# Optimization experiments

Hardware: AMD Instinct MI355X
Metric: run time of the kernel (lower is better)

Reference implementation:

```python
import jax, jax.numpy as jnp
import numpy as np

B, T, D, H = 8, 2048, 512, 128

def setup_inputs() -> dict:
    key = jax.random.key(0)
    ks = jax.random.split(key, 8)
    s = lambda fan_in: 1.0 / np.sqrt(fan_in)
    return {
        "x": jax.random.normal(ks[0], (B, T, D), jnp.float32),
        "prediction": jax.random.normal(ks[1], (B, T, D), jnp.float32),
        "Wq": jax.random.uniform(ks[2], (D, H), jnp.float32, -s(D), s(D)),
        "bq": jnp.zeros((H,), jnp.float32),
        "Wk": jax.random.uniform(ks[3], (D, H), jnp.float32, -s(D), s(D)),
        "bk": jnp.zeros((H,), jnp.float32),
        "Wv": jax.random.uniform(ks[4], (D, D), jnp.float32, -s(D), s(D)),
        "bv": jnp.zeros((D,), jnp.float32),
        "Wf": jax.random.uniform(ks[5], (2 * D, D), jnp.float32, -s(2 * D), s(2 * D)),
        "bf": jnp.zeros((D,), jnp.float32),
    }

def reference(x, prediction, Wq, bq, Wk, bk, Wv, bv, Wf, bf):
    # q,k: [B,T,H]; v: [B,T,D]
    q = jnp.einsum('btd,dh->bth', prediction, Wq) + bq
    k = jnp.einsum('btd,dh->bth', x, Wk) + bk
    v = jnp.einsum('btd,de->bte', x, Wv) + bv
    # unscaled attention scores [B,T,T]
    scores = jnp.einsum('bth,bsh->bts', q, k)
    attn = jax.nn.softmax(scores, axis=-1)
    attended = jnp.einsum('bts,bsd->btd', attn, v)
    fusion_input = jnp.concatenate([prediction, attended], axis=-1)  # [B,T,2D]
    return jax.nn.sigmoid(jnp.einsum('btf,fd->btd', fusion_input, Wf) + bf)
```

## Files before the change

kernel.cpp:

```cpp
#include <hip/hip_runtime.h>
#include <hip/hip_bf16.h>


#define APF_B 8
#define APF_T 2048
#define APF_D 512
#define APF_H 128
#define APF_M (APF_B * APF_T)

#define GSWZ(row) ((((row) >> 1) & 3) << 3)

typedef unsigned short u16;
typedef __attribute__((ext_vector_type(8))) short short8;
typedef __attribute__((ext_vector_type(4))) float f32x4;
typedef __attribute__((ext_vector_type(16))) float f32x16;

static __device__ __forceinline__ u16 f2bf(float x) {
    union { float f; unsigned int u; } cv;
    cv.f = x;
    unsigned int u = cv.u + 0x7FFFu + ((cv.u >> 16) & 1u);
    return (u16)(u >> 16);
}
static __device__ __forceinline__ u16 f2bf_hw(float x) {
    union { __hip_bfloat16 h; u16 u; } cv;
    cv.h = __float2bfloat16(x);
    return cv.u;
}

static __device__ __forceinline__ void load16_lds(const u16* g, u16* l) {
    __builtin_amdgcn_global_load_lds(
        (const __attribute__((address_space(1))) unsigned int*)g,
        (__attribute__((address_space(3))) unsigned int*)l,
        16, 0, 0);
}

template <int N>
static __device__ __forceinline__ void bar_keep() {
    if constexpr (N == 0)
        asm volatile("s_waitcnt vmcnt(0) lgkmcnt(0)\ns_barrier" ::: "memory");
    else if constexpr (N == 4)
        asm volatile("s_waitcnt vmcnt(4) lgkmcnt(0)\ns_barrier" ::: "memory");
    else if constexpr (N == 8)
        asm volatile("s_waitcnt vmcnt(8) lgkmcnt(0)\ns_barrier" ::: "memory");
}

static __device__ __forceinline__ f32x16 zero16() {
    f32x16 v;
#pragma unroll
    for (int i = 0; i < 16; ++i) v[i] = 0.f;
    return v;
}

__global__ __launch_bounds__(256) void prep_w(
    const float* __restrict__ Wq, u16* __restrict__ WqT,
    const float* __restrict__ Wk, u16* __restrict__ WkT,
    const float* __restrict__ Wv, u16* __restrict__ WvT,
    const float* __restrict__ Wf, u16* __restrict__ WfT)
{
    __shared__ float tile[64][65];
    int b = blockIdx.x;
    const float* src; u16* dst; int K, N;
    if (b < 16)      { src = Wq; dst = WqT; K = 512;  N = 128; }
    else if (b < 32) { b -= 16; src = Wk; dst = WkT; K = 512;  N = 128; }
    else if (b < 96) { b -= 32; src = Wv; dst = WvT; K = 512;  N = 512; }
    else             { b -= 96; src = Wf; dst = WfT; K = 1024; N = 512; }
    const int ntN = N >> 6;
    const int k0 = (b / ntN) * 64, n0 = (b % ntN) * 64;

    const int tid = threadIdx.x;
#pragma unroll
    for (int rep = 0; rep < 4; ++rep) {
        const int r = (tid >> 4) + rep * 16;
        const int c = (tid & 15) * 4;
        const float4 v = *(const float4*)&src[(long)(k0 + r) * N + n0 + c];
        tile[r][c] = v.x; tile[r][c + 1] = v.y;
        tile[r][c + 2] = v.z; tile[r][c + 3] = v.w;
    }
    __syncthreads();
#pragma unroll
    for (int rep = 0; rep < 2; ++rep) {
        const int rn = (tid >> 3) + rep * 32;
        const int ck = (tid & 7) * 8;
        short8 o;
#pragma unroll
        for (int j = 0; j < 8; ++j)
            o[j] = (short)f2bf_hw(tile[ck + j][rn]);
        *(short8*)&dst[(long)(n0 + rn) * K + k0 + ck] = o;
    }
}

template <int ADT, int BDT, int EPI, int BIASM, int VBLK>
static __device__ __forceinline__ void gemm_body(
    u16 (&smA)[2][4096], u16 (&smB)[2][4096],
    const void* Ap, long lda,
    const void* Bp, long ldb,
    const float* bias, void* Cp, long ldc, int K,
    long row0, long col0, const float* Cadd)
{
    const int tid  = threadIdx.x;
    const int lane = tid & 63;
    const int wid  = tid >> 6;
    const int wr   = wid >> 1;
    const int wc   = wid & 1;

    f32x4 acc[4][4];
#pragma unroll
    for (int i = 0; i < 4; ++i)
#pragma unroll
        for (int j = 0; j < 4; ++j)
            acc[i][j] = (f32x4){0.f, 0.f, 0.f, 0.f};

    const int lrow = (lane >> 4) * 4;
    const int lcol = lane & 15;
    const int q8   = (lane >> 4) * 8;

    float4 ra[2][2], rb[2][2];

    auto loadA = [&](int kb) {
        if (ADT == 1) {
            const float* Af = (const float*)Ap;
#pragma unroll
            for (int rep = 0; rep < 2; ++rep) {
                const int c = tid + rep * 256;
                const int rr = c >> 2, kc = (c & 3) * 8;
                const float* ga = Af + (row0 + rr) * lda + kb + kc;
                ra[rep][0] = *(const float4*)ga;
                ra[rep][1] = *(const float4*)(ga + 4);
            }
        }
    };
    auto loadB = [&](int kb) {
        if (BDT == 1) {
            const float* Bf = (const float*)Bp;
#pragma unroll
            for (int rep = 0; rep < 2; ++rep) {
                const int c = tid + rep * 256;
                const int rr = c >> 2, kc = (c & 3) * 8;
                const float* gb = Bf + (col0 + rr) * ldb + kb + kc;
                rb[rep][0] = *(const float4*)gb;
                rb[rep][1] = *(const float4*)(gb + 4);
            }
        }
    };
    auto dmaA = [&](int buf, int kb) {
        if (ADT == 0) {
            const u16* Ab = (const u16*)Ap;
#pragma unroll
            for (int rep = 0; rep < 2; ++rep) {
                const int c = tid + rep * 256;
                const int rr = c >> 2, kc = (c & 3) * 8;
                const int wbase = (wid * 64 + rep * 256) * 8;
                load16_lds(Ab + (row0 + rr) * lda + kb + (kc ^ GSWZ(rr)),
                           &smA[buf][wbase]);
            }
        }
    };
    auto dmaB = [&](int buf, int kb) {
        if (BDT == 0) {
            const u16* Bb = (const u16*)Bp;
#pragma unroll
            for (int rep = 0; rep < 2; ++rep) {
                const int c = tid + rep * 256;
                const int rr = c >> 2, kc = (c & 3) * 8;
                const int wbase = (wid * 64 + rep * 256) * 8;
                load16_lds(Bb + (col0 + rr) * ldb + kb + (kc ^ GSWZ(rr)),
                           &smB[buf][wbase]);
            }
        }
    };
    auto cvt8 = [&](const float4& a, const float4& b) {
        short8 v;
        v[0] = (short)f2bf_hw(a.x); v[1] = (short)f2bf_hw(a.y);
        v[2] = (short)f2bf_hw(a.z); v[3] = (short)f2bf_hw(a.w);
        v[4] = (short)f2bf_hw(b.x); v[5] = (short)f2bf_hw(b.y);
        v[6] = (short)f2bf_hw(b.z); v[7] = (short)f2bf_hw(b.w);
        return v;
    };
    auto writeA = [&](int buf) {
        if (ADT == 1) {
#pragma unroll
            for (int rep = 0; rep < 2; ++rep) {
                const int c = tid + rep * 256;
                *(short8*)&smA[buf][(c * 8) ^ GSWZ(c >> 2)] =
                    cvt8(ra[rep][0], ra[rep][1]);
            }
        }
    };
    auto writeB = [&](int buf) {
        if (BDT == 1) {
#pragma unroll
            for (int rep = 0; rep < 2; ++rep) {
                const int c = tid + rep * 256;
                *(short8*)&smB[buf][(c * 8) ^ GSWZ(c >> 2)] =
                    cvt8(rb[rep][0], rb[rep][1]);
            }
        }
    };

    constexpr int NREG = (ADT == 1 ? 4 : 0) + (BDT == 1 ? 4 : 0);

    const int NT = K / 32;
    loadA(0); loadB(0);
    writeA(0); writeB(0);
    dmaA(0, 0); dmaB(0, 0);

    int cur = 0;
    for (int t = 0; t < NT; ++t) {
        const int kb2 = (t + 1) * 32;
        if (t + 1 < NT) {
            loadA(kb2); loadB(kb2);
            bar_keep<NREG>();
            dmaA(cur ^ 1, kb2); dmaB(cur ^ 1, kb2);
        } else {
            bar_keep<0>();
        }

        short8 av[4], bv4[4];
#pragma unroll
        for (int ti = 0; ti < 4; ++ti) {
            const int arow = wr * 64 + ti * 16 + lcol;
            av[ti] = *(const short8*)&smA[cur][arow * 32 + (q8 ^ GSWZ(arow))];
        }
#pragma unroll
        for (int tj = 0; tj < 4; ++tj) {
            const int brow = wc * 64 + tj * 16 + lcol;
            bv4[tj] = *(const short8*)&smB[cur][brow * 32 + (q8 ^ GSWZ(brow))];
        }

#pragma unroll
        for (int ti = 0; ti < 4; ++ti)
#pragma unroll
            for (int tj = 0; tj < 4; ++tj)
                acc[ti][tj] = __builtin_amdgcn_mfma_f32_16x16x32_bf16(
                    av[ti], bv4[tj], acc[ti][tj], 0, 0, 0);

        if (t + 1 < NT) { writeA(cur ^ 1); writeB(cur ^ 1); }
        cur ^= 1;
    }

#pragma unroll
    for (int ti = 0; ti < 4; ++ti) {
        const long m0t = row0 + wr * 64 + ti * 16 + lrow;
#pragma unroll
        for (int tj = 0; tj < 4; ++tj) {
            const long n = col0 + wc * 64 + tj * 16 + lcol;
            const float bn = (BIASM == 0 && bias != nullptr) ? bias[n] : 0.f;
            if (EPI == 0) {
                u16* C = (u16*)Cp;
#pragma unroll
                for (int r = 0; r < 4; ++r) {
                    const long m = m0t + r;
                    const float bm = (BIASM == 1) ? bias[m] : bn;
                    long idx;
                    if (VBLK) {
                        idx = ((((m >> 5) * 256) + (n >> 3)) << 8) +
                              ((m & 31) << 3) + (n & 7);
                    } else {
                        idx = m * ldc + n;
                    }
                    C[idx] = f2bf(acc[ti][tj][r] + bm);
                }
            } else if (EPI == 2) {
                float* C = (float*)Cp;
#pragma unroll
                for (int r = 0; r < 4; ++r) {
                    const float val = acc[ti][tj][r] + bn;
                    C[(m0t + r) * ldc + n] = 1.0f / (1.0f + expf(-val));
                }
            } else if (EPI == 3) {
                float* C = (float*)Cp;
#pragma unroll
                for (int r = 0; r < 4; ++r)
                    C[(m0t + r) * ldc + n] = acc[ti][tj][r] + bn;
            } else {
                float* C = (float*)Cp;
#pragma unroll
                for (int r = 0; r < 4; ++r) {
                    const float val = acc[ti][tj][r] + Cadd[(m0t + r) * ldc + n];
                    C[(m0t + r) * ldc + n] = 1.0f / (1.0f + expf(-val));
                }
            }
        }
    }
}

__global__ __launch_bounds__(256, 3) void mid_gemms(
    const float* __restrict__ x, const float* __restrict__ pred,
    const u16* __restrict__ WqT, const u16* __restrict__ WkT,
    const u16* __restrict__ WvT, const u16* __restrict__ WfT,
    const float* __restrict__ bq, const float* __restrict__ bk,
    const float* __restrict__ bv, const float* __restrict__ bfu,
    u16* __restrict__ qb, u16* __restrict__ kbuf, u16* __restrict__ vTb,
    float* __restrict__ Cpre)
{
    __shared__ u16 smA[2][4096];
    __shared__ u16 smB[2][4096];

    const int bid = blockIdx.x;
    if (bid < 256) {
        const int zz = bid >> 7, by = bid & 127;
        gemm_body<1, 0, 0, 0, 0>(smA, smB,
            zz ? (const void*)x : (const void*)pred, APF_D,
            zz ? WkT : WqT, APF_D,
            zz ? bk : bq, zz ? (void*)kbuf : (void*)qb, APF_H, APF_D,
            (long)by * 128, 0, nullptr);
    } else if (bid < 768) {
        const int t = bid - 256;
        const int zz = t >> 6, rem = t & 63;
        const int bx = rem & 15, by = rem >> 4;
        gemm_body<0, 1, 0, 1, 1>(smA, smB,
            WvT, APF_D,
            (const void*)(x + (long)zz * APF_T * APF_D), APF_D,
            bv, (void*)(vTb + (long)zz * 1048576L), APF_T, APF_D,
            (long)by * 128, (long)bx * 128, nullptr);
    } else {
        const int t = bid - 768;
        const int bx = t & 3, by = t >> 2;
        gemm_body<1, 0, 3, 0, 0>(smA, smB,
            (const void*)pred, APF_D,
            WfT, 1024,
            bfu, (void*)Cpre, APF_D, APF_D,
            (long)by * 128, (long)bx * 128, nullptr);
    }
}

__global__ __launch_bounds__(256, 2) void fusion_gemm(
    const u16* __restrict__ attb, const u16* __restrict__ WfT,
    const float* __restrict__ Cpre, float* __restrict__ out)
{
    __shared__ u16 smA[2][4096];
    __shared__ u16 smB[2][4096];
    gemm_body<0, 0, 4, 0, 0>(smA, smB,
        (const void*)attb, APF_D,
        WfT + 512, 1024,
        nullptr, (void*)out, APF_D, APF_D,
        (long)blockIdx.y * 128, (long)blockIdx.x * 128, Cpre);
}

__global__ __launch_bounds__(256, 2) void attn_fused(
    const u16* __restrict__ qg, const u16* __restrict__ kg,
    const u16* __restrict__ vTg, u16* __restrict__ attg)
{
    __shared__ u16 sK[2][64 * 128];
    __shared__ u16 sP[2][64 * 64];
    __shared__ float sRS[192];

    const int tid  = threadIdx.x;
    const int lane = tid & 63;
    const int w    = tid >> 6;
    const int l31  = lane & 31;
    const int hi   = lane >> 5;
    const int qb   = w >> 1;
    const int sb   = w & 1;

    const int  bid = blockIdx.x;
    const long z   = bid & 7;
    const int  r   = bid >> 3;
    const long q0  = (long)(r & 31) * 64;
    const long d0  = (long)(r >> 5) * 256;

    const u16* kbase0 = kg + z * (long)APF_T * APF_H;

#pragma unroll
    for (int rep = 0; rep < 4; ++rep) {
        const int c    = tid + rep * 256;
        const int row  = c >> 4;
        const int col8 = (c & 15) * 8;
        load16_lds(kbase0 + row * APF_H + (col8 ^ ((row & 15) << 3)),
                   &sK[0][c * 8]);
    }

    short8 qf[8];
    {
        const u16* qsrc = qg + (z * APF_T + q0 + qb * 32 + l31) * APF_H;
#pragma unroll
        for (int ks = 0; ks < 8; ++ks)
            qf[ks] = *(const short8*)(qsrc + ks * 16 + hi * 8);
    }
    __syncthreads();

    f32x16 oacc[2][2];
#pragma unroll
    for (int i = 0; i < 2; ++i)
#pragma unroll
        for (int j = 0; j < 2; ++j) oacc[i][j] = zero16();
    f32x16 rsacc = zero16();

    const long dblk0 = (d0 >> 5) + w * 2;
    const u16* vzb = vTg + z * 1048576L + dblk0 * 65536L + (long)l31 * 8;

    const int krow = sb * 32 + l31;
    const int pcol = sb * 32 + l31;

    int cur = 0;
    for (int kt = 0; kt < APF_T / 64; ++kt) {
        asm volatile("s_waitcnt vmcnt(0)" ::: "memory");

        f32x16 sacc0 = zero16(), sacc1 = zero16();
#pragma unroll
        for (int ks = 0; ks < 4; ++ks) {
            const int c0 = (2 * ks) * 16 + hi * 8;
            const int c1 = (2 * ks + 1) * 16 + hi * 8;
            const short8 bv0 =
                *(const short8*)&sK[cur][krow * 128 + (c0 ^ ((krow & 15) << 3))];
            const short8 bv1 =
                *(const short8*)&sK[cur][krow * 128 + (c1 ^ ((krow & 15) << 3))];
            sacc0 = __builtin_amdgcn_mfma_f32_32x32x16_bf16(qf[2 * ks], bv0, sacc0, 0, 0, 0);
            sacc1 = __builtin_amdgcn_mfma_f32_32x32x16_bf16(qf[2 * ks + 1], bv1, sacc1, 0, 0, 0);
        }

        const long sbase = (long)kt * 8 + hi;
        short8 vf[2][4];
#pragma unroll
        for (int dt = 0; dt < 2; ++dt)
#pragma unroll
            for (int ks = 0; ks < 4; ++ks)
                vf[dt][ks] = *(const short8*)(vzb + dt * 65536L + (sbase + ks * 2) * 256);

        if (kt + 1 < APF_T / 64) {
            const u16* ksrc = kbase0 + (long)(kt + 1) * 64 * APF_H;
#pragma unroll
            for (int rep = 0; rep < 4; ++rep) {
                const int c    = tid + rep * 256;
                const int row  = c >> 4;
                const int col8 = (c & 15) * 8;
                load16_lds(ksrc + row * APF_H + (col8 ^ ((row & 15) << 3)),
                           &sK[cur ^ 1][c * 8]);
            }
        }

#pragma unroll
        for (int rg = 0; rg < 16; ++rg) {
            const float e = __expf(sacc0[rg] + sacc1[rg]);
            rsacc[rg] += e;
            const int prow = qb * 32 + (rg & 3) + 8 * (rg >> 2) + 4 * hi;
            sP[cur][prow * 64 + (pcol ^ ((prow & 7) << 3))] = f2bf(e);
        }
        asm volatile("s_waitcnt lgkmcnt(0)\ns_barrier" ::: "memory");

#pragma unroll
        for (int ks = 0; ks < 4; ++ks) {
            const int colk = ks * 16 + hi * 8;
            short8 pa[2];
#pragma unroll
            for (int qt = 0; qt < 2; ++qt) {
                const int prow = qt * 32 + l31;
                pa[qt] = *(const short8*)&sP[cur][prow * 64 + (colk ^ ((prow & 7) << 3))];
            }
#pragma unroll
            for (int dt = 0; dt < 2; ++dt)
#pragma unroll
                for (int qt = 0; qt < 2; ++qt)
                    oacc[qt][dt] = __builtin_amdgcn_mfma_f32_32x32x16_bf16(
                        pa[qt], vf[dt][ks], oacc[qt][dt], 0, 0, 0);
        }
        cur ^= 1;
    }

#pragma unroll
    for (int rg = 0; rg < 16; ++rg) {
        float s = rsacc[rg];
        s += __shfl_xor(s, 1);
        s += __shfl_xor(s, 2);
        s += __shfl_xor(s, 4);
        s += __shfl_xor(s, 8);
        s += __shfl_xor(s, 16);
        rsacc[rg] = s;
    }
    if (l31 == 0) {
#pragma unroll
        for (int rg = 0; rg < 16; ++rg) {
            const int row = (rg & 3) + 8 * (rg >> 2) + 4 * hi;
            sRS[w * 32 + row] = rsacc[rg];
        }
    }
    __syncthreads();
    if (tid < 64) {
        const int qb2 = tid >> 5, r2 = tid & 31;
        sRS[128 + tid] = 1.0f / (sRS[(qb2 * 2 + 0) * 32 + r2] +
                                 sRS[(qb2 * 2 + 1) * 32 + r2]);
    }
    __syncthreads();

    const long rowg0 = z * APF_T + q0;
    const long colg0 = d0 + (long)w * 64;
#pragma unroll
    for (int qt = 0; qt < 2; ++qt)
#pragma unroll
        for (int rg = 0; rg < 16; ++rg) {
            const int row = qt * 32 + (rg & 3) + 8 * (rg >> 2) + 4 * hi;
            const float inv = sRS[128 + row];
#pragma unroll
            for (int dt = 0; dt < 2; ++dt)
                attg[(rowg0 + row) * APF_D + colg0 + dt * 32 + l31] =
                    f2bf(oacc[qt][dt][rg] * inv);
        }
}

extern "C" void kernel_launch(void* const* d_in, const int* in_sizes, int n_in,
                              void* d_out, int out_size, void* d_ws, size_t ws_size,
                              hipStream_t stream)
{
    (void)in_sizes; (void)n_in; (void)out_size; (void)ws_size;

    const float* x    = (const float*)d_in[0];
    const float* pred = (const float*)d_in[1];
    const float* Wq   = (const float*)d_in[2];
    const float* bq   = (const float*)d_in[3];
    const float* Wk   = (const float*)d_in[4];
    const float* bk   = (const float*)d_in[5];
    const float* Wv   = (const float*)d_in[6];
    const float* bv   = (const float*)d_in[7];
    const float* Wf   = (const float*)d_in[8];
    const float* bfu  = (const float*)d_in[9];

    float* Cpre = (float*)d_ws;
    u16* wsp  = (u16*)(Cpre + (long)APF_M * APF_D);
    u16* qb   = wsp;
    u16* kbuf = qb   + (long)APF_M * APF_H;
    u16* vTb  = kbuf + (long)APF_M * APF_H;
    u16* attb = vTb  + (long)APF_M * APF_D;
    u16* WqT  = attb + (long)APF_M * APF_D;
    u16* WkT  = WqT  + (long)APF_H * APF_D;
    u16* WvT  = WkT  + (long)APF_H * APF_D;
    u16* WfT  = WvT  + (long)APF_D * APF_D;

    const dim3 thr(256);

    prep_w<<<dim3(224), thr, 0, stream>>>(Wq, WqT, Wk, WkT, Wv, WvT, Wf, WfT);

    mid_gemms<<<dim3(1280), thr, 0, stream>>>(
        x, pred, WqT, WkT, WvT, WfT, bq, bk, bv, bfu, qb, kbuf, vTb, Cpre);

    attn_fused<<<dim3(512), thr, 0, stream>>>(qb, kbuf, vTb, attb);

    fusion_gemm<<<dim3(4, 128), thr, 0, stream>>>(attb, WfT, Cpre,
                                                  (float*)d_out);
}
```

Measured before the change: 248.9 us.

## Restructure attention tiles to 32 queries by 128 keys with single-buffered K

The attention kernel now gives each block 32 query rows and each wave a distinct 32-key slice of a 128-key tile. K is single-buffered with an extra barrier, P goes through a padded LDS layout, and launch bounds rise to 3 blocks per CU over a doubled grid. This roughly halves the K-tile reuse per block, which doubles K reloads across blocks and loses the K prefetch overlap, in exchange for more parallelism and occupancy. The bf16 conversions also switch to the hardware intrinsic.

```diff
diff --git a/kernel.cpp b/kernel.cpp
--- a/kernel.cpp
+++ b/kernel.cpp
@@ -9,6 +9,7 @@
 #define APF_M (APF_B * APF_T)
 
 #define GSWZ(row) ((((row) >> 1) & 3) << 3)
+#define FA_LDP 132
 
 typedef unsigned short u16;
 typedef __attribute__((ext_vector_type(8))) short short8;
@@ -258,7 +259,7 @@
                     } else {
                         idx = m * ldc + n;
                     }
-                    C[idx] = f2bf(acc[ti][tj][r] + bm);
+                    C[idx] = f2bf_hw(acc[ti][tj][r] + bm);
                 }
             } else if (EPI == 2) {
                 float* C = (float*)Cp;
@@ -337,124 +338,120 @@
         (long)blockIdx.y * 128, (long)blockIdx.x * 128, Cpre);
 }
 
-__global__ __launch_bounds__(256, 2) void attn_fused(
+__global__ __launch_bounds__(256, 3) void attn_fused(
     const u16* __restrict__ qg, const u16* __restrict__ kg,
     const u16* __restrict__ vTg, u16* __restrict__ attg)
 {
-    __shared__ u16 sK[2][64 * 128];
-    __shared__ u16 sP[2][64 * 64];
-    __shared__ float sRS[192];
+    __shared__ u16 sK[128 * 128];
+    __shared__ u16 sP[32 * FA_LDP];
+    __shared__ float sRS[160];
 
     const int tid  = threadIdx.x;
     const int lane = tid & 63;
     const int w    = tid >> 6;
     const int l31  = lane & 31;
     const int hi   = lane >> 5;
-    const int qb   = w >> 1;
-    const int sb   = w & 1;
 
     const int  bid = blockIdx.x;
     const long z   = bid & 7;
-    const int  r   = bid >> 3;
-    const long q0  = (long)(r & 31) * 64;
-    const long d0  = (long)(r >> 5) * 256;
+    const long q0  = (long)((bid >> 3) & 63) * 32;
+    const long d0  = (long)(bid >> 9) * 256;
 
     const u16* kbase0 = kg + z * (long)APF_T * APF_H;
 
 #pragma unroll
-    for (int rep = 0; rep < 4; ++rep) {
+    for (int rep = 0; rep < 8; ++rep) {
         const int c    = tid + rep * 256;
         const int row  = c >> 4;
         const int col8 = (c & 15) * 8;
         load16_lds(kbase0 + row * APF_H + (col8 ^ ((row & 15) << 3)),
-                   &sK[0][c * 8]);
+                   &sK[c * 8]);
     }
 
     short8 qf[8];
     {
-        const u16* qsrc = qg + (z * APF_T + q0 + qb * 32 + l31) * APF_H;
+        const u16* qsrc = qg + (z * APF_T + q0 + l31) * APF_H;
 #pragma unroll
         for (int ks = 0; ks < 8; ++ks)
             qf[ks] = *(const short8*)(qsrc + ks * 16 + hi * 8);
     }
-    __syncthreads();
-
-    f32x16 oacc[2][2];
-#pragma unroll
-    for (int i = 0; i < 2; ++i)
-#pragma unroll
-        for (int j = 0; j < 2; ++j) oacc[i][j] = zero16();
+
+    f32x16 oacc[2];
+    oacc[0] = zero16(); oacc[1] = zero16();
     f32x16 rsacc = zero16();
 
     const long dblk0 = (d0 >> 5) + w * 2;
     const u16* vzb = vTg + z * 1048576L + dblk0 * 65536L + (long)l31 * 8;
 
-    const int krow = sb * 32 + l31;
-    const int pcol = sb * 32 + l31;
-
-    int cur = 0;
-    for (int kt = 0; kt < APF_T / 64; ++kt) {
-        asm volatile("s_waitcnt vmcnt(0)" ::: "memory");
-
-        f32x16 sacc0 = zero16(), sacc1 = zero16();
-#pragma unroll
-        for (int ks = 0; ks < 4; ++ks) {
-            const int c0 = (2 * ks) * 16 + hi * 8;
-            const int c1 = (2 * ks + 1) * 16 + hi * 8;
-            const short8 bv0 =
-                *(const short8*)&sK[cur][krow * 128 + (c0 ^ ((krow & 15) << 3))];
-            const short8 bv1 =
-                *(const short8*)&sK[cur][krow * 128 + (c1 ^ ((krow & 15) << 3))];
-            sacc0 = __builtin_amdgcn_mfma_f32_32x32x16_bf16(qf[2 * ks], bv0, sacc0, 0, 0, 0);
-            sacc1 = __builtin_amdgcn_mfma_f32_32x32x16_bf16(qf[2 * ks + 1], bv1, sacc1, 0, 0, 0);
-        }
-
-        const long sbase = (long)kt * 8 + hi;
-        short8 vf[2][4];
+    const int krow = w * 32 + l31;
+    const int pcol = w * 32 + l31;
+
+    for (int kt = 0; kt < APF_T / 128; ++kt) {
+        asm volatile("s_waitcnt vmcnt(0)\ns_barrier" ::: "memory");
+
+        f32x16 sacc = zero16();
+#pragma unroll
+        for (int ks = 0; ks < 8; ++ks) {
+            const int colk = ks * 16 + hi * 8;
+            const short8 bv =
+                *(const short8*)&sK[krow * 128 + (colk ^ ((krow & 15) << 3))];
+            sacc = __builtin_amdgcn_mfma_f32_32x32x16_bf16(qf[ks], bv, sacc, 0, 0, 0);
+        }
+
+        const long sbase = (long)kt * 16 + hi;
+        short8 vf1[2][4];
 #pragma unroll
         for (int dt = 0; dt < 2; ++dt)
 #pragma unroll
             for (int ks = 0; ks < 4; ++ks)
-                vf[dt][ks] = *(const short8*)(vzb + dt * 65536L + (sbase + ks * 2) * 256);
-
-        if (kt + 1 < APF_T / 64) {
-            const u16* ksrc = kbase0 + (long)(kt + 1) * 64 * APF_H;
-#pragma unroll
-            for (int rep = 0; rep < 4; ++rep) {
+                vf1[dt][ks] = *(const short8*)(vzb + dt * 65536L + (sbase + ks * 2) * 256);
+
+#pragma unroll
+        for (int rg = 0; rg < 16; ++rg) {
+            const float e = __expf(sacc[rg]);
+            rsacc[rg] += e;
+            const int prow = (rg & 3) + 8 * (rg >> 2) + 4 * hi;
+            sP[prow * FA_LDP + pcol] = f2bf_hw(e);
+        }
+        asm volatile("s_waitcnt lgkmcnt(0)\ns_barrier" ::: "memory");
+
+        if (kt + 1 < APF_T / 128) {
+            const u16* ksrc = kbase0 + (long)(kt + 1) * 128 * APF_H;
+#pragma unroll
+            for (int rep = 0; rep < 8; ++rep) {
                 const int c    = tid + rep * 256;
                 const int row  = c >> 4;
                 const int col8 = (c & 15) * 8;
                 load16_lds(ksrc + row * APF_H + (col8 ^ ((row & 15) << 3)),
-                           &sK[cur ^ 1][c * 8]);
-            }
-        }
-
-#pragma unroll
-        for (int rg = 0; rg < 16; ++rg) {
-            const float e = __expf(sacc0[rg] + sacc1[rg]);
-            rsacc[rg] += e;
-            const int prow = qb * 32 + (rg & 3) + 8 * (rg >> 2) + 4 * hi;
-            sP[cur][prow * 64 + (pcol ^ ((prow & 7) << 3))] = f2bf(e);
-        }
-        asm volatile("s_waitcnt lgkmcnt(0)\ns_barrier" ::: "memory");
+                           &sK[c * 8]);
+            }
+        }
 
 #pragma unroll
         for (int ks = 0; ks < 4; ++ks) {
             const int colk = ks * 16 + hi * 8;
-            short8 pa[2];
-#pragma unroll
-            for (int qt = 0; qt < 2; ++qt) {
-                const int prow = qt * 32 + l31;
-                pa[qt] = *(const short8*)&sP[cur][prow * 64 + (colk ^ ((prow & 7) << 3))];
-            }
+            const short8 pa = *(const short8*)&sP[l31 * FA_LDP + colk];
 #pragma unroll
             for (int dt = 0; dt < 2; ++dt)
-#pragma unroll
-                for (int qt = 0; qt < 2; ++qt)
-                    oacc[qt][dt] = __builtin_amdgcn_mfma_f32_32x32x16_bf16(
-                        pa[qt], vf[dt][ks], oacc[qt][dt], 0, 0, 0);
-        }
-        cur ^= 1;
+                oacc[dt] = __builtin_amdgcn_mfma_f32_32x32x16_bf16(
+                    pa, vf1[dt][ks], oacc[dt], 0, 0, 0);
+        }
+
+        short8 vf2[2][4];
+#pragma unroll
+        for (int dt = 0; dt < 2; ++dt)
+#pragma unroll
+            for (int ks = 0; ks < 4; ++ks)
+                vf2[dt][ks] = *(const short8*)(vzb + dt * 65536L + (sbase + 8 + ks * 2) * 256);
+#pragma unroll
+        for (int ks = 0; ks < 4; ++ks) {
+            const int colk = (ks + 4) * 16 + hi * 8;
+            const short8 pa = *(const short8*)&sP[l31 * FA_LDP + colk];
+#pragma unroll
+            for (int dt = 0; dt < 2; ++dt)
+                oacc[dt] = __builtin_amdgcn_mfma_f32_32x32x16_bf16(
+                    pa, vf2[dt][ks], oacc[dt], 0, 0, 0);
+        }
     }
 
 #pragma unroll
@@ -475,26 +472,23 @@
         }
     }
     __syncthreads();
-    if (tid < 64) {
-        const int qb2 = tid >> 5, r2 = tid & 31;
-        sRS[128 + tid] = 1.0f / (sRS[(qb2 * 2 + 0) * 32 + r2] +
-                                 sRS[(qb2 * 2 + 1) * 32 + r2]);
+    if (tid < 32) {
+        sRS[128 + tid] = 1.0f / (sRS[tid] + sRS[32 + tid] +
+                                 sRS[64 + tid] + sRS[96 + tid]);
     }
     __syncthreads();
 
     const long rowg0 = z * APF_T + q0;
     const long colg0 = d0 + (long)w * 64;
 #pragma unroll
-    for (int qt = 0; qt < 2; ++qt)
-#pragma unroll
-        for (int rg = 0; rg < 16; ++rg) {
-            const int row = qt * 32 + (rg & 3) + 8 * (rg >> 2) + 4 * hi;
-            const float inv = sRS[128 + row];
-#pragma unroll
-            for (int dt = 0; dt < 2; ++dt)
-                attg[(rowg0 + row) * APF_D + colg0 + dt * 32 + l31] =
-                    f2bf(oacc[qt][dt][rg] * inv);
-        }
+    for (int rg = 0; rg < 16; ++rg) {
+        const int row = (rg & 3) + 8 * (rg >> 2) + 4 * hi;
+        const float inv = sRS[128 + row];
+#pragma unroll
+        for (int dt = 0; dt < 2; ++dt)
+            attg[(rowg0 + row) * APF_D + colg0 + dt * 32 + l31] =
+                f2bf_hw(oacc[dt][rg] * inv);
+    }
 }
 
 extern "C" void kernel_launch(void* const* d_in, const int* in_sizes, int n_in,
@@ -532,7 +526,7 @@
     mid_gemms<<<dim3(1280), thr, 0, stream>>>(
         x, pred, WqT, WkT, WvT, WfT, bq, bk, bv, bfu, qb, kbuf, vTb, Cpre);
 
-    attn_fused<<<dim3(512), thr, 0, stream>>>(qb, kbuf, vTb, attb);
+    attn_fused<<<dim3(1024), thr, 0, stream>>>(qb, kbuf, vTb, attb);
 
     fusion_gemm<<<dim3(4, 128), thr, 0, stream>>>(attb, WfT, Cpre,
                                                   (float*)d_out);
```

Result: slower. 312.9 us (+25.7%).
